# Performance work log

Hardware: AMD Instinct MI355X
Metric: run time of the kernel (lower is better)

Reference implementation:

```python
import jax, jax.numpy as jnp
import numpy as np

D_MODEL = 2048
NUM_HEADS = 16
D_K = D_MODEL // NUM_HEADS  # 128
THETA = 10000.0
B, S = 4, 2048


def _apply_rope(t, token_positions, theta=THETA):
    # t: [B, H, S, d_k]; rotate interleaved (even, odd) pairs
    d_k = t.shape[-1]
    inv_freq = 1.0 / (theta ** (jnp.arange(0, d_k, 2, dtype=jnp.float32) / d_k))  # [d_k/2]
    angles = token_positions.astype(jnp.float32)[:, None] * inv_freq[None, :]     # [S, d_k/2]
    cos = jnp.cos(angles)  # [S, d_k/2]
    sin = jnp.sin(angles)
    t1 = t[..., 0::2]  # [B,H,S,d_k/2]
    t2 = t[..., 1::2]
    r1 = t1 * cos - t2 * sin
    r2 = t1 * sin + t2 * cos
    out = jnp.stack([r1, r2], axis=-1)  # [B,H,S,d_k/2,2]
    return out.reshape(t.shape)


def setup_inputs() -> dict:
    key = jax.random.key(0)
    ks = jax.random.split(key, 5)
    scale = 0.02
    return {
        "x": jax.random.normal(ks[0], (B, S, D_MODEL), dtype=jnp.float32),
        "token_positions": jnp.arange(S, dtype=jnp.int64 if jax.config.jax_enable_x64 else jnp.int32),
        "Wq": jax.random.normal(ks[1], (D_MODEL, D_MODEL), dtype=jnp.float32) * scale,
        "Wk": jax.random.normal(ks[2], (D_MODEL, D_MODEL), dtype=jnp.float32) * scale,
        "Wv": jax.random.normal(ks[3], (D_MODEL, D_MODEL), dtype=jnp.float32) * scale,
        "Wo": jax.random.normal(ks[4], (D_MODEL, D_MODEL), dtype=jnp.float32) * scale,
    }


def reference(x, token_positions, Wq, Wk, Wv, Wo):
    # Linear(in, out): weight [out, in], y = x @ W.T (no bias)
    q = jnp.einsum('bsd,ed->bse', x, Wq)
    k = jnp.einsum('bsd,ed->bse', x, Wk)
    v = jnp.einsum('bsd,ed->bse', x, Wv)
    # split heads: [B, S, H*dk] -> [B, H, S, dk]
    def split(t):
        return t.reshape(B, S, NUM_HEADS, D_K).transpose(0, 2, 1, 3)
    qh, kh, vh = split(q), split(k), split(v)
    qh = _apply_rope(qh, token_positions)
    kh = _apply_rope(kh, token_positions)
    scores = jnp.einsum('bhqd,bhkd->bhqk', qh, kh) / jnp.sqrt(jnp.float32(D_K))
    causal = jnp.tril(jnp.ones((S, S), dtype=bool))
    scores = jnp.where(causal[None, None], scores, jnp.finfo(scores.dtype).min)
    attn = jax.nn.softmax(scores, axis=-1)
    attended = jnp.einsum('bhqk,bhkd->bhqd', attn, vh)  # [B,H,S,dk]
    merged = attended.transpose(0, 2, 1, 3).reshape(B, S, D_MODEL)
    return jnp.einsum('bsd,ed->bse', merged, Wo)
```

## Files before the change

### kernel.cpp

```cpp
#include <hip/hip_runtime.h>
#include <stdint.h>


using u16 = unsigned short;
typedef __bf16 bf16_t;
typedef __bf16 bf16x8 __attribute__((ext_vector_type(8)));
typedef float  f32x4  __attribute__((ext_vector_type(4)));
typedef u16    u16x4  __attribute__((ext_vector_type(4)));

#define DEVI static __device__ __forceinline__
#define AS1 __attribute__((address_space(1)))
#define AS3 __attribute__((address_space(3)))
#define GLL16(g,l) __builtin_amdgcn_global_load_lds((const AS1 void*)(g), (AS3 void*)(l), 16, 0, 0)

DEVI u16 f2bf(float x){ bf16_t h=(bf16_t)x; return __builtin_bit_cast(u16,h); }
DEVI f32x4 mfma16(bf16x8 a, bf16x8 b, f32x4 c){
  return __builtin_amdgcn_mfma_f32_16x16x32_bf16(a,b,c,0,0,0);
}

__global__ __launch_bounds__(256) void k_cvt(const float* __restrict__ in, u16* __restrict__ out){
  int i = blockIdx.x*256 + threadIdx.x;
  float4 v = ((const float4*)in)[i];
  u16x4 o = { f2bf(v.x), f2bf(v.y), f2bf(v.z), f2bf(v.w) };
  ((u16x4*)out)[i] = o;
}

__global__ __launch_bounds__(256) void k_tab(const int* __restrict__ pos, float* __restrict__ ct, float* __restrict__ stab){
  int i = blockIdx.x*256 + threadIdx.x;
  int s = i>>6, f = i&63;
  float inv = __expf(-0.14391275442161033f * (float)f);
  float a = (float)pos[s] * inv;
  float sv, cv; sincosf(a, &sv, &cv);
  ct[i] = cv; stab[i] = sv;
}

template<int EPI>
__global__ __launch_bounds__(512,2) void k_gemm(
    const bf16_t* __restrict__ A, const bf16_t* __restrict__ Bt,
    void* __restrict__ O0, void* __restrict__ O1, void* __restrict__ O2,
    const float* __restrict__ ct, const float* __restrict__ stab)
{
  __shared__ char Al[2][32768];
  __shared__ char Bl[2][2][16384];
  const int tid = threadIdx.x, wave = tid>>6, lane = tid&63;
  const int rgrp = lane>>4, cidx = lane&15;
  const int wm = wave>>2, wn = wave&3;
  const int xcd = blockIdx.x & 7, ii = blockIdx.x >> 3;
  const int by = xcd*4 + (ii&3), bx = ii>>2;
  const int bm = by*256, bn = bx*256;

  const char* Ag = (const char*)A  + (size_t)bm*4096;
  const char* Bg = (const char*)Bt + (size_t)bn*4096;

  const int a_r  = lane>>3;
  const int a_src = ((lane&7)*16) ^ ((a_r&7)<<4);
  const int b_r  = lane>>2;
  const int b_src = ((lane&3)*16) ^ ((b_r&6)<<3);
  const int aswz = (cidx&7)<<4;
  const int bswz = (cidx&6)<<3;

  f32x4 acc[2][4][4] = {};
  bf16x8 af[4], bfA[4], bfB[4];

#define STAGE_A(b, kt_, mh) do{ _Pragma("unroll") \
  for (int c_=0;c_<2;++c_){ \
    const int r0_ = c_*128 + (mh)*64 + wave*8; \
    GLL16(Ag + (size_t)(r0_ + a_r)*4096 + (size_t)(kt_)*128 + a_src, \
          &Al[b][r0_*128]); } }while(0)
#define STAGE_B(b, kt_, kk) do{ _Pragma("unroll") \
  for (int c_=0;c_<2;++c_){ \
    const int r0_ = c_*128 + wave*16; \
    GLL16(Bg + (size_t)(r0_ + b_r)*4096 + (size_t)(kt_)*128 + (kk)*64 + b_src, \
          &Bl[b][kk][r0_*64]); } }while(0)
#define LOAD_AF(MH, KK) do{ _Pragma("unroll") \
  for (int fi=0; fi<4; ++fi) \
    af[fi] = *(const bf16x8*)&Al[cur][(wm*128 + (MH)*64 + fi*16 + cidx)*128 \
                                      + (((KK)*64 + rgrp*16) ^ aswz)]; }while(0)
#define LOAD_BF(DST, KK) do{ _Pragma("unroll") \
  for (int fj=0; fj<4; ++fj) \
    DST[fj] = *(const bf16x8*)&Bl[cur][KK][(wn*64 + fj*16 + cidx)*64 \
                                      + ((rgrp*16) ^ bswz)]; }while(0)
#define PHASE_MFMA(ACCI, BFR) do{ \
  __builtin_amdgcn_s_barrier(); \
  asm volatile("s_waitcnt lgkmcnt(0)" ::: "memory"); \
  __builtin_amdgcn_sched_barrier(0); \
  __builtin_amdgcn_s_setprio(1); \
  _Pragma("unroll") for (int fi=0; fi<4; ++fi){ \
    _Pragma("unroll") for (int fj=0; fj<4; ++fj){ \
      acc[ACCI][fi][fj] = mfma16(af[fi], BFR[fj], acc[ACCI][fi][fj]); }} \
  __builtin_amdgcn_s_setprio(0); }while(0)
#define VMC(n) asm volatile("s_waitcnt vmcnt(" #n ")" ::: "memory")

  STAGE_A(0, 0, 0); STAGE_B(0, 0, 0); STAGE_A(0, 0, 1); STAGE_B(0, 0, 1);
  VMC(4);
  __builtin_amdgcn_s_barrier();
  int cur = 0;
  for (int t=0; t<32; ++t){
    const bool pf = (t < 31);
    LOAD_AF(0,0); LOAD_BF(bfA, 0);
    if (pf){ STAGE_A(cur^1, t+1, 0); VMC(4); } else VMC(2);
    PHASE_MFMA(0, bfA);
    LOAD_AF(1,0);
    if (pf){ STAGE_B(cur^1, t+1, 0); VMC(4); } else VMC(0);
    PHASE_MFMA(1, bfA);
    LOAD_AF(0,1); LOAD_BF(bfB, 1);
    if (pf) STAGE_A(cur^1, t+1, 1);
    PHASE_MFMA(0, bfB);
    LOAD_AF(1,1);
    if (pf){ STAGE_B(cur^1, t+1, 1); VMC(4); }
    PHASE_MFMA(1, bfB);
    cur ^= 1;
  }
#undef STAGE_A
#undef STAGE_B
#undef LOAD_AF
#undef LOAD_BF
#undef PHASE_MFMA
#undef VMC

  if constexpr (EPI==3){
    float* O = (float*)O0;
    #pragma unroll
    for (int mh=0; mh<2; ++mh)
      #pragma unroll
      for (int fi=0; fi<4; ++fi){
        const int m0 = bm + wm*128 + mh*64 + fi*16 + rgrp*4;
        #pragma unroll
        for (int fj=0; fj<4; ++fj){
          const int n = bn + wn*64 + fj*16 + cidx;
          #pragma unroll
          for (int r=0; r<4; ++r)
            O[(size_t)(m0+r)*2048 + n] = acc[mh][fi][fj][r];
        }
      }
  } else {
    const int seg = bn>>11;
    if (seg==2){
      u16* O = (u16*)O2;
      #pragma unroll
      for (int mh=0; mh<2; ++mh)
        #pragma unroll
        for (int fi=0; fi<4; ++fi){
          const int m0 = bm + wm*128 + mh*64 + fi*16 + rgrp*4;
          const int b = m0>>11, s0 = m0&2047;
          #pragma unroll
          for (int fj=0; fj<4; ++fj){
            const int nl = (bn + wn*64 + fj*16 + cidx) & 2047;
            const int h = nl>>7, d = nl&127;
            u16x4 pk = { f2bf(acc[mh][fi][fj][0]), f2bf(acc[mh][fi][fj][1]),
                         f2bf(acc[mh][fi][fj][2]), f2bf(acc[mh][fi][fj][3]) };
            *(u16x4*)(O + ((size_t)((b*16+h)*128 + d)*2048 + s0)) = pk;
          }
        }
    } else {
      u16* O = seg ? (u16*)O1 : (u16*)O0;
      const float qs = seg ? 1.0f : 0.08838834764831845f;
      #pragma unroll
      for (int fj=0; fj<4; ++fj){
        const int nl = (bn + wn*64 + fj*16 + cidx) & 2047;
        const int h = nl>>7, d = nl&127, f = (nl&127)>>1;
        #pragma unroll
        for (int mh=0; mh<2; ++mh)
          #pragma unroll
          for (int fi=0; fi<4; ++fi){
            #pragma unroll
            for (int r=0; r<4; ++r){
              const int m = bm + wm*128 + mh*64 + fi*16 + rgrp*4 + r;
              const int b = m>>11, s = m&2047;
              float v = acc[mh][fi][fj][r];
              float p = __shfl_xor(v, 1, 64);
              float cv = ct[s*64+f], sv = stab[s*64+f];
              float o = (d&1) ? (p*sv + v*cv) : (v*cv - p*sv);
              o *= qs;
              O[(size_t)(b*16+h)*262144 + (size_t)s*128 + d] = f2bf(o);
            }
          }
      }
    }
  }
}

__global__ __launch_bounds__(256,2) void k_attn(
  const bf16_t* __restrict__ Q, const bf16_t* __restrict__ K,
  const bf16_t* __restrict__ Vt, u16* __restrict__ Mg)
{
  __shared__ char kl[2][16384];
  __shared__ char vl[2][16384];
  __shared__ char pl[4][4096];
  const int tid=threadIdx.x, wave=tid>>6, lane=tid&63;
  const int rgrp=lane>>4, cidx=lane&15;
  const int bid=blockIdx.x;
  const int qt = 15 - (bid>>6);
  const int bh = bid & 63;
  const int qbase = qt*128;
  const int last = 2*qt + 1;

  bf16x8 qf[2][4];
  #pragma unroll
  for (int m=0;m<2;++m){
    const bf16_t* qp = Q + ((size_t)bh*2048 + qbase + wave*32 + m*16 + cidx)*128 + rgrp*8;
    #pragma unroll
    for (int ds=0; ds<4; ++ds) qf[m][ds] = *(const bf16x8*)(qp + ds*32);
  }
  f32x4 oacc[2][8] = {};
  float mrow[2] = {-1e30f,-1e30f};
  float lrow[2] = {0.f,0.f};

  const char* Kg = (const char*)K  + (size_t)bh*524288;
  const char* Vg = (const char*)Vt + (size_t)bh*524288;
  char* pw = pl[wave];
  const int L0 = tid*16;
  const int qrow0 = qbase + wave*32 + cidx;

  #define STAGE(buf, kt_) do{                                                  \
    _Pragma("unroll")                                                          \
    for (int i_=0;i_<4;++i_){                                                  \
      int L_ = i_*4096 + L0;                                                   \
      int row_ = L_>>8;                                                        \
      int in_ = (L_&255) ^ ((row_&7)<<4);                                      \
      GLL16(Kg + (size_t)((kt_)*64+row_)*256 + in_, &kl[buf][i_*4096 + wave*1024]); \
    }                                                                          \
    _Pragma("unroll")                                                          \
    for (int i_=0;i_<4;++i_){                                                  \
      int L_ = i_*4096 + L0;                                                   \
      int d_ = L_>>7;                                                          \
      int in_ = (L_&127) ^ ((d_&7)<<4);                                        \
      GLL16(Vg + (size_t)d_*4096 + (kt_)*128 + in_, &vl[buf][i_*4096 + wave*1024]); \
    }                                                                          \
  }while(0)

  STAGE(0, 0);
  int cur = 0;
  for (int kt=0; kt<=last; ++kt){
    const bool pf = (kt < last);
    if (pf) STAGE(cur^1, kt+1);
    if (pf) asm volatile("s_waitcnt vmcnt(8)" ::: "memory");
    else    asm volatile("s_waitcnt vmcnt(0)" ::: "memory");
    __builtin_amdgcn_s_barrier();

    f32x4 stt[2][4];
    #pragma unroll
    for (int m=0;m<2;++m)
      #pragma unroll
      for (int t=0;t<4;++t) stt[m][t] = (f32x4){0.f,0.f,0.f,0.f};
    __builtin_amdgcn_s_setprio(1);
    #pragma unroll
    for (int t=0;t<4;++t){
      const int krow = t*16 + cidx;
      #pragma unroll
      for (int ds=0; ds<4; ++ds){
        const int off = (krow*256 + ds*64 + rgrp*16) ^ ((krow&7)<<4);
        bf16x8 kf = *(const bf16x8*)(&kl[cur][off]);
        stt[0][t] = mfma16(kf, qf[0][ds], stt[0][t]);
        stt[1][t] = mfma16(kf, qf[1][ds], stt[1][t]);
      }
    }
    __builtin_amdgcn_s_setprio(0);

    if (kt >= 2*qt){
      #pragma unroll
      for (int m=0;m<2;++m){
        const int q = qrow0 + m*16;
        #pragma unroll
        for (int t=0;t<4;++t){
          #pragma unroll
          for (int r=0;r<4;++r){
            const int key = kt*64 + t*16 + rgrp*4 + r;
            if (key > q) stt[m][t][r] = -1e30f;
          }
        }
      }
    }

    #pragma unroll
    for (int m=0;m<2;++m){
      float vm = stt[m][0][0];
      #pragma unroll
      for (int t=0;t<4;++t)
        #pragma unroll
        for (int r=0;r<4;++r) vm = fmaxf(vm, stt[m][t][r]);
      vm = fmaxf(vm, __shfl_xor(vm, 16, 64));
      vm = fmaxf(vm, __shfl_xor(vm, 32, 64));
      if (!__all(vm <= mrow[m] + 8.f)){
        float mn = fmaxf(mrow[m], vm);
        float c = __expf(mrow[m]-mn);
        mrow[m]=mn; lrow[m]*=c;
        float cr0 = __shfl(c, rgrp*4+0, 64), cr1 = __shfl(c, rgrp*4+1, 64);
        float cr2 = __shfl(c, rgrp*4+2, 64), cr3 = __shfl(c, rgrp*4+3, 64);
        #pragma unroll
        for (int d=0;d<8;++d){
          oacc[m][d][0]*=cr0; oacc[m][d][1]*=cr1;
          oacc[m][d][2]*=cr2; oacc[m][d][3]*=cr3;
        }
      }
      float lt = 0.f;
      #pragma unroll
      for (int t=0;t<4;++t)
        #pragma unroll
        for (int r=0;r<4;++r){
          float p = __expf(stt[m][t][r]-mrow[m]);
          stt[m][t][r]=p; lt+=p;
        }
      lt += __shfl_xor(lt, 16, 64);
      lt += __shfl_xor(lt, 32, 64);
      lrow[m] += lt;
    }

    #pragma unroll
    for (int m=0;m<2;++m){
      const int prow = m*16 + cidx;
      char* base = pw + prow*128;
      const int swz = (prow&7)<<4;
      #pragma unroll
      for (int t=0;t<4;++t){
        u16x4 pk = { f2bf(stt[m][t][0]), f2bf(stt[m][t][1]), f2bf(stt[m][t][2]), f2bf(stt[m][t][3]) };
        *(u16x4*)(base + ((t*32 + rgrp*8) ^ swz)) = pk;
      }
    }
    asm volatile("s_waitcnt lgkmcnt(0)" ::: "memory");
    __builtin_amdgcn_sched_barrier(0);

    __builtin_amdgcn_s_setprio(1);
    #pragma unroll
    for (int ks=0; ks<2; ++ks){
      const int swzc = (cidx&7)<<4;
      bf16x8 pa0 = *(const bf16x8*)(pw + (     cidx)*128 + ((ks*64 + rgrp*16) ^ swzc));
      bf16x8 pa1 = *(const bf16x8*)(pw + (16 + cidx)*128 + ((ks*64 + rgrp*16) ^ swzc));
      #pragma unroll
      for (int dsub=0; dsub<8; ++dsub){
        const int d = dsub*16 + cidx;
        const int off = (d*128 + ks*64 + rgrp*16) ^ ((d&7)<<4);
        bf16x8 vf = *(const bf16x8*)(&vl[cur][off]);
        oacc[0][dsub] = mfma16(pa0, vf, oacc[0][dsub]);
        oacc[1][dsub] = mfma16(pa1, vf, oacc[1][dsub]);
      }
    }
    __builtin_amdgcn_s_setprio(0);
    __builtin_amdgcn_s_barrier();
    cur ^= 1;
  }
  #undef STAGE

  const int b = bh>>4, h = bh&15;
  #pragma unroll
  for (int m=0;m<2;++m){
    float linv = 1.f/lrow[m];
    float ir[4];
    #pragma unroll
    for (int r=0;r<4;++r) ir[r] = __shfl(linv, rgrp*4+r, 64);
    #pragma unroll
    for (int dsub=0;dsub<8;++dsub){
      const int col = h*128 + dsub*16 + cidx;
      #pragma unroll
      for (int r=0;r<4;++r){
        const int srow = qbase + wave*32 + m*16 + rgrp*4 + r;
        Mg[((size_t)b*2048 + srow)*2048 + col] = f2bf(oacc[m][dsub][r]*ir[r]);
      }
    }
  }
}

extern "C" void kernel_launch(void* const* d_in, const int* in_sizes, int n_in,
                              void* d_out, int out_size, void* d_ws, size_t ws_size,
                              hipStream_t stream)
{
  (void)in_sizes; (void)n_in; (void)out_size; (void)ws_size;
  const float* x  = (const float*)d_in[0];
  const int*   tp = (const int*)d_in[1];
  const float* Wq = (const float*)d_in[2];
  const float* Wk = (const float*)d_in[3];
  const float* Wv = (const float*)d_in[4];
  const float* Wo = (const float*)d_in[5];

  char* ws = (char*)d_ws;
  bf16_t* xb  = (bf16_t*)(ws);
  bf16_t* wqb = (bf16_t*)(ws + 33554432);
  bf16_t* wkb = (bf16_t*)(ws + 41943040);
  bf16_t* wvb = (bf16_t*)(ws + 50331648);
  bf16_t* wob = (bf16_t*)(ws + 58720256);
  bf16_t* vt  = (bf16_t*)(ws + 67108864);
  float*  ct  = (float*) (ws + 100663296);
  float*  stb = (float*) (ws + 101187584);
  bf16_t* qr  = (bf16_t*)d_out;
  bf16_t* kr  = (bf16_t*)((char*)d_out + 33554432);
  bf16_t* mg  = xb;

  k_cvt<<<16384,256,0,stream>>>(x,  (u16*)xb);
  k_cvt<<< 4096,256,0,stream>>>(Wq, (u16*)wqb);
  k_cvt<<< 4096,256,0,stream>>>(Wk, (u16*)wkb);
  k_cvt<<< 4096,256,0,stream>>>(Wv, (u16*)wvb);
  k_cvt<<< 4096,256,0,stream>>>(Wo, (u16*)wob);
  k_tab<<<  512,256,0,stream>>>(tp, ct, stb);

  k_gemm<4><<<768,512,0,stream>>>(xb, wqb, qr, kr, vt, ct, stb);
  k_attn<<<1024,256,0,stream>>>(qr, kr, vt, (u16*)mg);
  k_gemm<3><<<256,512,0,stream>>>(mg, wob, d_out, nullptr, nullptr, nullptr, nullptr);
}
```

Baseline: 394.9 us.

## Restructure GEMM main loop into two phases and merge weight conversions

Reworks the GEMM K-loop. All four global-to-LDS stages for the next tile are issued up front, then each K-half loads all A and B fragments into separate registers and runs 32 MFMAs per phase, so there are fewer barriers and waitcnt points per iteration. This trades finer-grained interleaving of loads and MFMAs for fewer synchronisations, at the cost of more fragment registers. It also fuses the four weight-conversion launches into one kernel to cut launch overhead. There is a redundant repeated LOAD_AF(af0,0,0) in the new loop.

```diff
diff --git a/kernel.cpp b/kernel.cpp
--- a/kernel.cpp
+++ b/kernel.cpp
@@ -23,6 +23,18 @@
   float4 v = ((const float4*)in)[i];
   u16x4 o = { f2bf(v.x), f2bf(v.y), f2bf(v.z), f2bf(v.w) };
   ((u16x4*)out)[i] = o;
+}
+
+__global__ __launch_bounds__(256) void k_cvtw(
+    const float* __restrict__ w0, const float* __restrict__ w1,
+    const float* __restrict__ w2, const float* __restrict__ w3,
+    u16* __restrict__ out){
+  const int seg = blockIdx.x >> 12;
+  const float* w = (seg==0)? w0 : (seg==1)? w1 : (seg==2)? w2 : w3;
+  int i = (blockIdx.x & 4095)*256 + threadIdx.x;
+  float4 v = ((const float4*)w)[i];
+  u16x4 o = { f2bf(v.x), f2bf(v.y), f2bf(v.z), f2bf(v.w) };
+  ((u16x4*)(out + (size_t)seg*4194304))[i] = o;
 }
 
 __global__ __launch_bounds__(256) void k_tab(const int* __restrict__ pos, float* __restrict__ ct, float* __restrict__ stab){
@@ -60,7 +72,7 @@
   const int bswz = (cidx&6)<<3;
 
   f32x4 acc[2][4][4] = {};
-  bf16x8 af[4], bfA[4], bfB[4];
+  bf16x8 af0[4], af1[4], bfA[4], bfB[4];
 
 #define STAGE_A(b, kt_, mh) do{ _Pragma("unroll") \
   for (int c_=0;c_<2;++c_){ \
@@ -72,50 +84,59 @@
     const int r0_ = c_*128 + wave*16; \
     GLL16(Bg + (size_t)(r0_ + b_r)*4096 + (size_t)(kt_)*128 + (kk)*64 + b_src, \
           &Bl[b][kk][r0_*64]); } }while(0)
-#define LOAD_AF(MH, KK) do{ _Pragma("unroll") \
+#define LOAD_AF(DST, MH, KK) do{ _Pragma("unroll") \
   for (int fi=0; fi<4; ++fi) \
-    af[fi] = *(const bf16x8*)&Al[cur][(wm*128 + (MH)*64 + fi*16 + cidx)*128 \
+    DST[fi] = *(const bf16x8*)&Al[cur][(wm*128 + (MH)*64 + fi*16 + cidx)*128 \
                                       + (((KK)*64 + rgrp*16) ^ aswz)]; }while(0)
 #define LOAD_BF(DST, KK) do{ _Pragma("unroll") \
   for (int fj=0; fj<4; ++fj) \
     DST[fj] = *(const bf16x8*)&Bl[cur][KK][(wn*64 + fj*16 + cidx)*64 \
                                       + ((rgrp*16) ^ bswz)]; }while(0)
-#define PHASE_MFMA(ACCI, BFR) do{ \
-  __builtin_amdgcn_s_barrier(); \
-  asm volatile("s_waitcnt lgkmcnt(0)" ::: "memory"); \
-  __builtin_amdgcn_sched_barrier(0); \
-  __builtin_amdgcn_s_setprio(1); \
-  _Pragma("unroll") for (int fi=0; fi<4; ++fi){ \
-    _Pragma("unroll") for (int fj=0; fj<4; ++fj){ \
-      acc[ACCI][fi][fj] = mfma16(af[fi], BFR[fj], acc[ACCI][fi][fj]); }} \
-  __builtin_amdgcn_s_setprio(0); }while(0)
 #define VMC(n) asm volatile("s_waitcnt vmcnt(" #n ")" ::: "memory")
 
   STAGE_A(0, 0, 0); STAGE_B(0, 0, 0); STAGE_A(0, 0, 1); STAGE_B(0, 0, 1);
-  VMC(4);
+  VMC(0);
   __builtin_amdgcn_s_barrier();
   int cur = 0;
   for (int t=0; t<32; ++t){
     const bool pf = (t < 31);
-    LOAD_AF(0,0); LOAD_BF(bfA, 0);
-    if (pf){ STAGE_A(cur^1, t+1, 0); VMC(4); } else VMC(2);
-    PHASE_MFMA(0, bfA);
-    LOAD_AF(1,0);
-    if (pf){ STAGE_B(cur^1, t+1, 0); VMC(4); } else VMC(0);
-    PHASE_MFMA(1, bfA);
-    LOAD_AF(0,1); LOAD_BF(bfB, 1);
-    if (pf) STAGE_A(cur^1, t+1, 1);
-    PHASE_MFMA(0, bfB);
-    LOAD_AF(1,1);
-    if (pf){ STAGE_B(cur^1, t+1, 1); VMC(4); }
-    PHASE_MFMA(1, bfB);
+    if (pf){
+      STAGE_A(cur^1, t+1, 0); STAGE_B(cur^1, t+1, 0);
+      STAGE_A(cur^1, t+1, 1); STAGE_B(cur^1, t+1, 1);
+      VMC(8);
+    } else VMC(0);
+    __builtin_amdgcn_sched_barrier(0);
+    LOAD_AF(af0, 0, 0); LOAD_AF(af1, 1, 0); LOAD_BF(bfA, 0);
+    LOAD_AF(af0, 0, 0);
+    asm volatile("s_waitcnt lgkmcnt(0)" ::: "memory");
+    __builtin_amdgcn_sched_barrier(0);
+    __builtin_amdgcn_s_barrier();
+    __builtin_amdgcn_s_setprio(1);
+    _Pragma("unroll") for (int fi=0; fi<4; ++fi)
+      _Pragma("unroll") for (int fj=0; fj<4; ++fj)
+        acc[0][fi][fj] = mfma16(af0[fi], bfA[fj], acc[0][fi][fj]);
+    _Pragma("unroll") for (int fi=0; fi<4; ++fi)
+      _Pragma("unroll") for (int fj=0; fj<4; ++fj)
+        acc[1][fi][fj] = mfma16(af1[fi], bfA[fj], acc[1][fi][fj]);
+    __builtin_amdgcn_s_setprio(0);
+    LOAD_AF(af0, 0, 1); LOAD_AF(af1, 1, 1); LOAD_BF(bfB, 1);
+    asm volatile("s_waitcnt lgkmcnt(0)" ::: "memory");
+    __builtin_amdgcn_sched_barrier(0);
+    __builtin_amdgcn_s_setprio(1);
+    _Pragma("unroll") for (int fi=0; fi<4; ++fi)
+      _Pragma("unroll") for (int fj=0; fj<4; ++fj)
+        acc[0][fi][fj] = mfma16(af0[fi], bfB[fj], acc[0][fi][fj]);
+    _Pragma("unroll") for (int fi=0; fi<4; ++fi)
+      _Pragma("unroll") for (int fj=0; fj<4; ++fj)
+        acc[1][fi][fj] = mfma16(af1[fi], bfB[fj], acc[1][fi][fj]);
+    __builtin_amdgcn_s_setprio(0);
+    __builtin_amdgcn_s_barrier();
     cur ^= 1;
   }
 #undef STAGE_A
 #undef STAGE_B
 #undef LOAD_AF
 #undef LOAD_BF
-#undef PHASE_MFMA
 #undef VMC
 
   if constexpr (EPI==3){
@@ -375,22 +396,17 @@
   char* ws = (char*)d_ws;
   bf16_t* xb  = (bf16_t*)(ws);
   bf16_t* wqb = (bf16_t*)(ws + 33554432);
-  bf16_t* wkb = (bf16_t*)(ws + 41943040);
-  bf16_t* wvb = (bf16_t*)(ws + 50331648);
-  bf16_t* wob = (bf16_t*)(ws + 58720256);
   bf16_t* vt  = (bf16_t*)(ws + 67108864);
   float*  ct  = (float*) (ws + 100663296);
   float*  stb = (float*) (ws + 101187584);
+  bf16_t* wob = (bf16_t*)(ws + 58720256);
   bf16_t* qr  = (bf16_t*)d_out;
   bf16_t* kr  = (bf16_t*)((char*)d_out + 33554432);
   bf16_t* mg  = xb;
 
-  k_cvt<<<16384,256,0,stream>>>(x,  (u16*)xb);
-  k_cvt<<< 4096,256,0,stream>>>(Wq, (u16*)wqb);
-  k_cvt<<< 4096,256,0,stream>>>(Wk, (u16*)wkb);
-  k_cvt<<< 4096,256,0,stream>>>(Wv, (u16*)wvb);
-  k_cvt<<< 4096,256,0,stream>>>(Wo, (u16*)wob);
-  k_tab<<<  512,256,0,stream>>>(tp, ct, stb);
+  k_cvt <<<16384,256,0,stream>>>(x, (u16*)xb);
+  k_cvtw<<<16384,256,0,stream>>>(Wq, Wk, Wv, Wo, (u16*)wqb);
+  k_tab <<<  512,256,0,stream>>>(tp, ct, stb);
 
   k_gemm<4><<<768,512,0,stream>>>(xb, wqb, qr, kr, vt, ct, stb);
   k_attn<<<1024,256,0,stream>>>(qr, kr, vt, (u16*)mg);
```

Result: slower. 472.5 us (+19.7%).
